# Optimization experiments

Measured on AMD Instinct MI355X. Metric: run time of the kernel, lower is better.

## Reference

```python
import jax, jax.numpy as jnp
import numpy as np

B, P, F = 128, 196, 2048   # batch, num_pixels, feature_dim
E, H, V = 512, 512, 10000  # embed_dim, hidden_dim, vocab_size
T = 32                     # max caption length


def setup_inputs() -> dict:
    key = jax.random.key(0)
    ks = jax.random.split(key, 12)
    s_e, s_h, s_f = 1.0 / np.sqrt(E), 1.0 / np.sqrt(H), 1.0 / np.sqrt(F)
    return {
        "features": jax.random.normal(ks[0], (B, P, F), jnp.float32),
        "captions": jax.random.randint(ks[1], (B, T), 0, V),
        # embedding table (init uniform(-0.1, 0.1) in the original)
        "emb_W": jax.random.uniform(ks[2], (V, E), jnp.float32, -0.1, 0.1),
        # LSTMCell params (PyTorch layout: [4H, in] with gate order i,f,g,o)
        "W_ih": jax.random.uniform(ks[3], (4 * H, E), jnp.float32, -s_h, s_h),
        "W_hh": jax.random.uniform(ks[4], (4 * H, H), jnp.float32, -s_h, s_h),
        "b_ih": jax.random.uniform(ks[5], (4 * H,), jnp.float32, -s_h, s_h),
        "b_hh": jax.random.uniform(ks[6], (4 * H,), jnp.float32, -s_h, s_h),
        # init_h / init_c linear layers: feature_dim -> hidden_dim
        "Wh": jax.random.uniform(ks[7], (H, F), jnp.float32, -s_f, s_f),
        "bh": jax.random.uniform(ks[8], (H,), jnp.float32, -s_f, s_f),
        "Wc": jax.random.uniform(ks[9], (H, F), jnp.float32, -s_f, s_f),
        "bc": jax.random.uniform(ks[10], (H,), jnp.float32, -s_f, s_f),
        # output projection (uniform(-0.1, 0.1) weights, zero bias)
        "fc_W": jax.random.uniform(ks[11], (V, H), jnp.float32, -0.1, 0.1),
        "fc_b": jnp.zeros((V,), jnp.float32),
    }


def _decode(features, captions, emb_W, W_ih, W_hh, b_ih, b_hh, Wh, bh, Wc, bc, fc_W, fc_b):
    # init hidden state from mean pooled features
    mean_feat = features.mean(axis=1)                       # [B, F]
    h0 = mean_feat @ Wh.T + bh                              # [B, H]
    c0 = mean_feat @ Wc.T + bc                              # [B, H]

    embeds = emb_W[captions]                                # [B, T, E]
    # x-side gate preactivations for all steps at once: [T-1, B, 4H]
    x_gates = jnp.einsum('bte,ge->tbg', embeds[:, :-1, :], W_ih) + (b_ih + b_hh)

    def step(carry, xg):
        h, c = carry
        gates = xg + h @ W_hh.T                             # [B, 4H]
        i, f, g, o = jnp.split(gates, 4, axis=-1)
        i, f, o = jax.nn.sigmoid(i), jax.nn.sigmoid(f), jax.nn.sigmoid(o)
        g = jnp.tanh(g)
        c_new = f * c + i * g
        h_new = o * jnp.tanh(c_new)
        return (h_new, c_new), h_new

    _, hs = jax.lax.scan(step, (h0, c0), x_gates)           # hs: [T-1, B, H]
    hs = jnp.swapaxes(hs, 0, 1)                             # [B, T-1, H]
    # dropout is identity in eval mode; fc applied per step == batched matmul
    return jnp.einsum('bth,vh->btv', hs, fc_W) + fc_b       # [B, T-1, V]


def reference(features, captions, emb_W, W_ih, W_hh, b_ih, b_hh, Wh, bh, Wc, bc, fc_W, fc_b):
    return _decode(features, captions, emb_W, W_ih, W_hh, b_ih, b_hh, Wh, bh, Wc, bc, fc_W, fc_b)
```

## Files before the change

kernel.cpp:

```cpp
#include <hip/hip_runtime.h>
#include <hip/hip_bf16.h>
#include <cstddef>

#define Bz 128
#define Pz 196
#define Fz 2048
#define Ez 512
#define Hz 512
#define Vz 10000
#define Tz 32
#define TM 31
#define Mrows (Bz * TM)
#define G4 (4 * Hz)
#define NPAD 10112

typedef __attribute__((ext_vector_type(8))) short bf16x8;
typedef __attribute__((ext_vector_type(4))) float f32x4;

__device__ __forceinline__ void gload_lds16(const void* g, void* l) {
    __builtin_amdgcn_global_load_lds(
        (const __attribute__((address_space(1))) unsigned int*)g,
        (__attribute__((address_space(3))) unsigned int*)l, 16, 0, 0);
}
__device__ __forceinline__ ushort f2b(float x) {
    __hip_bfloat16 b = __float2bfloat16(x);
    return *reinterpret_cast<ushort*>(&b);
}
__device__ __forceinline__ float b2f(ushort u) {
    __hip_bfloat16 b = *reinterpret_cast<__hip_bfloat16*>(&u);
    return __bfloat162float(b);
}

__global__ __launch_bounds__(256) void meanpool(const float* __restrict__ feat,
                                                float* __restrict__ mean) {
    int idx = blockIdx.x * 256 + threadIdx.x;
    int b = idx >> 9;
    int q = idx & 511;
    const float4* base = reinterpret_cast<const float4*>(feat) +
                         (size_t)b * Pz * (Fz / 4) + q;
    float4 acc = {0.f, 0.f, 0.f, 0.f};
    for (int p = 0; p < Pz; ++p) {
        float4 v = base[(size_t)p * (Fz / 4)];
        acc.x += v.x; acc.y += v.y; acc.z += v.z; acc.w += v.w;
    }
    const float s = 1.0f / (float)Pz;
    acc.x *= s; acc.y *= s; acc.z *= s; acc.w *= s;
    reinterpret_cast<float4*>(mean)[idx] = acc;
}

__global__ __launch_bounds__(256) void gather_cvt_emb(const float* __restrict__ emb,
                                                      const int* __restrict__ cap,
                                                      ushort* __restrict__ out) {
    int idx = blockIdx.x * 256 + threadIdx.x;
    if (idx >= Mrows * (Ez / 4)) return;
    int m = idx >> 7, kq = idx & 127;
    int b = m / TM;
    int t = m - b * TM;
    int row = cap[b * Tz + t];
    float4 v = reinterpret_cast<const float4*>(emb + (size_t)row * Ez)[kq];
    ushort4 o = {f2b(v.x), f2b(v.y), f2b(v.z), f2b(v.w)};
    reinterpret_cast<ushort4*>(out + (size_t)m * Ez)[kq] = o;
}

__global__ __launch_bounds__(256) void permute_wih(const float* __restrict__ W,
                                                   const float* __restrict__ b1,
                                                   const float* __restrict__ b2,
                                                   ushort* __restrict__ WP,
                                                   float* __restrict__ bP) {
    int idx = blockIdx.x * 256 + threadIdx.x;
    int o = idx >> 7, kq = idx & 127;
    int j = o >> 2, g = o & 3;
    int in = g * Hz + j;
    float4 v = reinterpret_cast<const float4*>(W + (size_t)in * Ez)[kq];
    ushort4 u = {f2b(v.x), f2b(v.y), f2b(v.z), f2b(v.w)};
    reinterpret_cast<ushort4*>(WP + (size_t)o * Ez)[kq] = u;
    if (kq == 0) bP[o] = b1[in] + b2[in];
}

__global__ __launch_bounds__(256) void permute_whh(const float* __restrict__ W,
                                                   ushort* __restrict__ Whi) {
    int idx = blockIdx.x * 256 + threadIdx.x;
    int o = idx >> 7, kq = idx & 127;
    int j = o >> 2, g = o & 3;
    int in = g * Hz + j;
    float4 v = reinterpret_cast<const float4*>(W + (size_t)in * Hz)[kq];
    ushort4 h = {f2b(v.x), f2b(v.y), f2b(v.z), f2b(v.w)};
    reinterpret_cast<ushort4*>(Whi + (size_t)o * Hz)[kq] = h;
}

__global__ __launch_bounds__(256) void cvt_bf16_pad4(const float* __restrict__ s,
                                                     ushort* __restrict__ d,
                                                     int n4src, int n4dst) {
    int i = blockIdx.x * 256 + threadIdx.x;
    if (i >= n4dst) return;
    ushort4 o;
    if (i < n4src) {
        float4 v = reinterpret_cast<const float4*>(s)[i];
        o.x = f2b(v.x); o.y = f2b(v.y); o.z = f2b(v.z); o.w = f2b(v.w);
    } else {
        o.x = o.y = o.z = o.w = 0;
    }
    reinterpret_cast<ushort4*>(d)[i] = o;
}

__global__ __launch_bounds__(256) void initk(
    const float* __restrict__ mean,
    const float* __restrict__ Wh, const float* __restrict__ Wc,
    float* __restrict__ partial)
{
    __shared__ float As[64][33];
    __shared__ float Bs2[64][33];
    const int n0 = blockIdx.x * 64;
    const int m0 = blockIdx.y * 64;
    const int kz = blockIdx.z;
    const int tid = threadIdx.x;
    const int tx = tid & 15, ty = tid >> 4;
    float acc[4][4] = {};

    for (int k0 = kz * 256; k0 < kz * 256 + 256; k0 += 32) {
#pragma unroll
        for (int i = 0; i < 2; ++i) {
            int e  = tid + i * 256;
            int r  = e >> 3;
            int cc = (e & 7) << 2;
            float4 va = *reinterpret_cast<const float4*>(
                mean + (size_t)(m0 + r) * Fz + k0 + cc);
            As[r][cc + 0] = va.x; As[r][cc + 1] = va.y;
            As[r][cc + 2] = va.z; As[r][cc + 3] = va.w;
            int n = n0 + r;
            const float* Brow = (n < Hz) ? (Wh + (size_t)n * Fz)
                                         : (Wc + (size_t)(n - Hz) * Fz);
            float4 vb = *reinterpret_cast<const float4*>(Brow + k0 + cc);
            Bs2[r][cc + 0] = vb.x; Bs2[r][cc + 1] = vb.y;
            Bs2[r][cc + 2] = vb.z; Bs2[r][cc + 3] = vb.w;
        }
        __syncthreads();
#pragma unroll
        for (int kk = 0; kk < 32; ++kk) {
            float a[4], bb[4];
#pragma unroll
            for (int i = 0; i < 4; ++i) a[i] = As[ty * 4 + i][kk];
#pragma unroll
            for (int j = 0; j < 4; ++j) bb[j] = Bs2[tx * 4 + j][kk];
#pragma unroll
            for (int i = 0; i < 4; ++i)
#pragma unroll
                for (int j = 0; j < 4; ++j)
                    acc[i][j] += a[i] * bb[j];
        }
        __syncthreads();
    }
#pragma unroll
    for (int i = 0; i < 4; ++i)
#pragma unroll
        for (int j = 0; j < 4; ++j)
            partial[((size_t)kz * 128 + m0 + ty * 4 + i) * 1024 + n0 + tx * 4 + j]
                = acc[i][j];
}

__global__ __launch_bounds__(256) void init_reduce(
    const float* __restrict__ partial,
    const float* __restrict__ bh, const float* __restrict__ bc,
    ushort* __restrict__ haHi, ushort* __restrict__ haLo,
    float* __restrict__ c0f)
{
    int idx = blockIdx.x * 256 + threadIdx.x;
    if (idx >= 128 * 1024) return;
    int m = idx >> 10, n = idx & 1023;
    float s = 0.f;
#pragma unroll
    for (int z = 0; z < 8; ++z)
        s += partial[((size_t)z * 128 + m) * 1024 + n];
    if (n < Hz) {
        s += bh[n];
        ushort hh = f2b(s);
        haHi[(size_t)m * Hz + n] = hh;
        haLo[(size_t)m * Hz + n] = f2b(s - b2f(hh));
    } else {
        c0f[(size_t)m * Hz + (n - Hz)] = s + bc[n - Hz];
    }
}

__global__ __launch_bounds__(256) void gemm_mfma(
    const ushort* __restrict__ A,
    const ushort* __restrict__ B,
    const float* __restrict__ bias,
    float* __restrict__ C,
    int Nb, int ldc, int K)
{
    __shared__ short Al[128 * 32];
    __shared__ short Bl[128 * 32];
    const int tid  = threadIdx.x;
    const int w    = tid >> 6;
    const int lane = tid & 63;

    const int nwg  = gridDim.x * gridDim.y;
    int orig = blockIdx.y * gridDim.x + blockIdx.x;
    int q = nwg >> 3, r = nwg & 7;
    int xcd = orig & 7, local = orig >> 3;
    int wgid = (xcd < r ? xcd * (q + 1) : r * (q + 1) + (xcd - r) * q) + local;
    const int m0 = (wgid / gridDim.x) * 128;
    const int n0 = (wgid % gridDim.x) * 128;
    const int wr = w >> 1, wc = w & 1;

    f32x4 acc[4][4] = {};

    const int srow = w * 32 + (lane >> 2);
    const int scol = (lane & 3) * 16;
    const char* Ag = (const char*)(A + (size_t)(m0 + srow) * K) + scol;
    const char* Bg = (const char*)(B + (size_t)(n0 + srow) * K) + scol;
    const size_t rstep = (size_t)16 * K * 2;
    short* Alb = Al + (w * 32) * 32;
    short* Blb = Bl + (w * 32) * 32;

    const int ko = (lane >> 4) * 8;
    const int fr = lane & 15;

    for (int k0 = 0; k0 < K; k0 += 32) {
        const size_t kb = (size_t)k0 * 2;
        gload_lds16(Ag + kb,         Alb);
        gload_lds16(Ag + kb + rstep, Alb + 16 * 32);
        gload_lds16(Bg + kb,         Blb);
        gload_lds16(Bg + kb + rstep, Blb + 16 * 32);
        __syncthreads();

        bf16x8 af[4], bf[4];
#pragma unroll
        for (int i = 0; i < 4; ++i)
            af[i] = *reinterpret_cast<const bf16x8*>(&Al[(wr * 64 + i * 16 + fr) * 32 + ko]);
#pragma unroll
        for (int j = 0; j < 4; ++j)
            bf[j] = *reinterpret_cast<const bf16x8*>(&Bl[(wc * 64 + j * 16 + fr) * 32 + ko]);
#pragma unroll
        for (int i = 0; i < 4; ++i)
#pragma unroll
            for (int j = 0; j < 4; ++j)
                acc[i][j] = __builtin_amdgcn_mfma_f32_16x16x32_bf16(
                    af[i], bf[j], acc[i][j], 0, 0, 0);
        __syncthreads();
    }

    const int r0 = (lane >> 4) * 4;
#pragma unroll
    for (int i = 0; i < 4; ++i) {
        int row = m0 + wr * 64 + i * 16 + r0;
#pragma unroll
        for (int j = 0; j < 4; ++j) {
            int col = n0 + wc * 64 + j * 16 + fr;
            if (col < Nb) {
                float bb = bias ? bias[col] : 0.f;
#pragma unroll
                for (int rr = 0; rr < 4; ++rr)
                    C[(size_t)(row + rr) * ldc + col] = acc[i][j][rr] + bb;
            }
        }
    }
}

__global__ __launch_bounds__(128) void lstm_step2(
    const float* __restrict__ xg,
    const ushort* __restrict__ Whi,
    const ushort* __restrict__ Ah,  const ushort* __restrict__ Alo,
    ushort* __restrict__ Oh, ushort* __restrict__ Ol,
    float* __restrict__ cst, ushort* __restrict__ hsb, int t)
{
    __shared__ float Cl[64][17];

    const int tid  = threadIdx.x;
    const int w    = tid >> 6;
    const int lane = tid & 63;
    const int fr   = lane & 15;
    const int hi4  = lane >> 4;
    const int n0   = blockIdx.x * 16;
    const int j0   = n0 >> 2;
    const int mb   = blockIdx.y * 64;
    const int m0w  = mb + w * 32;

    f32x4 acc[2] = {};

    const ushort* Bp  = Whi + (size_t)(n0 + fr) * Hz;
    const ushort* Ap0 = Ah  + (size_t)(m0w + fr) * Hz;
    const ushort* Ap1 = Ah  + (size_t)(m0w + 16 + fr) * Hz;
    const ushort* Lp0 = Alo + (size_t)(m0w + fr) * Hz;
    const ushort* Lp1 = Alo + (size_t)(m0w + 16 + fr) * Hz;

#pragma unroll
    for (int kc = 0; kc < 16; ++kc) {
        const size_t koff = (size_t)kc * 32 + hi4 * 8;
        bf16x8 bv  = *reinterpret_cast<const bf16x8*>(Bp  + koff);
        bf16x8 ah0 = *reinterpret_cast<const bf16x8*>(Ap0 + koff);
        bf16x8 ah1 = *reinterpret_cast<const bf16x8*>(Ap1 + koff);
        bf16x8 al0 = *reinterpret_cast<const bf16x8*>(Lp0 + koff);
        bf16x8 al1 = *reinterpret_cast<const bf16x8*>(Lp1 + koff);
        acc[0] = __builtin_amdgcn_mfma_f32_16x16x32_bf16(ah0, bv, acc[0], 0, 0, 0);
        acc[1] = __builtin_amdgcn_mfma_f32_16x16x32_bf16(ah1, bv, acc[1], 0, 0, 0);
        acc[0] = __builtin_amdgcn_mfma_f32_16x16x32_bf16(al0, bv, acc[0], 0, 0, 0);
        acc[1] = __builtin_amdgcn_mfma_f32_16x16x32_bf16(al1, bv, acc[1], 0, 0, 0);
    }

#pragma unroll
    for (int i = 0; i < 2; ++i)
#pragma unroll
        for (int r = 0; r < 4; ++r)
            Cl[w * 32 + i * 16 + hi4 * 4 + r][fr] = acc[i][r];
    __syncthreads();

    {
        const int lm = tid >> 1;
        const int m  = mb + lm;
        const int hp = (tid & 1) * 2;
        const float* xr = xg + ((size_t)m * TM + t) * G4 + n0 + 4 * hp;
        float4 x0 = *reinterpret_cast<const float4*>(xr);
        float4 x1 = *reinterpret_cast<const float4*>(xr + 4);
        float2 cc = *reinterpret_cast<const float2*>(cst + (size_t)m * Hz + j0 + hp);

        float gi0 = Cl[lm][4 * hp + 0] + x0.x;
        float gf0 = Cl[lm][4 * hp + 1] + x0.y;
        float gg0 = Cl[lm][4 * hp + 2] + x0.z;
        float go0 = Cl[lm][4 * hp + 3] + x0.w;
        float gi1 = Cl[lm][4 * hp + 4] + x1.x;
        float gf1 = Cl[lm][4 * hp + 5] + x1.y;
        float gg1 = Cl[lm][4 * hp + 6] + x1.z;
        float go1 = Cl[lm][4 * hp + 7] + x1.w;

        float i0 = 1.f / (1.f + expf(-gi0));
        float f0 = 1.f / (1.f + expf(-gf0));
        float g0 = tanhf(gg0);
        float o0 = 1.f / (1.f + expf(-go0));
        float i1 = 1.f / (1.f + expf(-gi1));
        float f1 = 1.f / (1.f + expf(-gf1));
        float g1 = tanhf(gg1);
        float o1 = 1.f / (1.f + expf(-go1));

        float cn0 = f0 * cc.x + i0 * g0;
        float cn1 = f1 * cc.y + i1 * g1;
        float h0v = o0 * tanhf(cn0);
        float h1v = o1 * tanhf(cn1);

        float2 cno = {cn0, cn1};
        *reinterpret_cast<float2*>(cst + (size_t)m * Hz + j0 + hp) = cno;

        ushort hh0 = f2b(h0v), hh1 = f2b(h1v);
        ushort hl0 = f2b(h0v - b2f(hh0)), hl1 = f2b(h1v - b2f(hh1));
        uint uh = (uint)hh0 | ((uint)hh1 << 16);
        uint ul = (uint)hl0 | ((uint)hl1 << 16);
        *reinterpret_cast<uint*>(Oh + (size_t)m * Hz + j0 + hp) = uh;
        *reinterpret_cast<uint*>(Ol + (size_t)m * Hz + j0 + hp) = ul;
        *reinterpret_cast<uint*>(hsb + ((size_t)m * TM + t) * Hz + j0 + hp) = uh;
    }
}

extern "C" void kernel_launch(void* const* d_in, const int* in_sizes, int n_in,
                              void* d_out, int out_size, void* d_ws, size_t ws_size,
                              hipStream_t stream) {
    const float* features = (const float*)d_in[0];
    const int*   captions = (const int*)d_in[1];
    const float* emb_W    = (const float*)d_in[2];
    const float* W_ih     = (const float*)d_in[3];
    const float* W_hh     = (const float*)d_in[4];
    const float* b_ih     = (const float*)d_in[5];
    const float* b_hh     = (const float*)d_in[6];
    const float* Wh       = (const float*)d_in[7];
    const float* bh       = (const float*)d_in[8];
    const float* Wc       = (const float*)d_in[9];
    const float* bc       = (const float*)d_in[10];
    const float* fc_W     = (const float*)d_in[11];
    const float* fc_b     = (const float*)d_in[12];
    float* out = (float*)d_out;

    float* w    = (float*)d_ws;
    float* mean = w;
    float* xg   = mean + Bz * Fz;
    float* partial = xg;
    float* c0f  = xg + (size_t)Mrows * G4;
    float* bP   = c0f + Bz * Hz;
    ushort* embg = (ushort*)(bP + G4);
    ushort* WihP = embg + (size_t)Mrows * Ez;
    ushort* Whi  = WihP + (size_t)G4 * Ez;
    ushort* fcWb = Whi + (size_t)G4 * Hz;
    ushort* hsb  = fcWb + (size_t)NPAD * Hz;
    ushort* haHi = hsb + (size_t)Mrows * Hz;
    ushort* haLo = haHi + Bz * Hz;
    ushort* hbHi = haLo + Bz * Hz;
    ushort* hbLo = hbHi + Bz * Hz;

    meanpool<<<(Bz * Fz / 4) / 256, 256, 0, stream>>>(features, mean);
    gather_cvt_emb<<<(Mrows * (Ez / 4) + 255) / 256, 256, 0, stream>>>(emb_W, captions, embg);
    permute_wih<<<(G4 * (Ez / 4)) / 256, 256, 0, stream>>>(W_ih, b_ih, b_hh, WihP, bP);
    permute_whh<<<(G4 * (Hz / 4)) / 256, 256, 0, stream>>>(W_hh, Whi);
    cvt_bf16_pad4<<<(NPAD * Hz / 4 + 255) / 256, 256, 0, stream>>>(
        fc_W, fcWb, Vz * Hz / 4, NPAD * Hz / 4);

    initk<<<dim3(16, 2, 8), 256, 0, stream>>>(mean, Wh, Wc, partial);
    init_reduce<<<(128 * 1024) / 256, 256, 0, stream>>>(
        partial, bh, bc, haHi, haLo, c0f);

    gemm_mfma<<<dim3(G4 / 128, Mrows / 128), 256, 0, stream>>>(
        embg, WihP, bP, xg, G4, G4, Ez);

    for (int t = 0; t < TM; ++t) {
        const ushort* ih = (t & 1) ? hbHi : haHi;
        const ushort* il = (t & 1) ? hbLo : haLo;
        ushort* oh = (t & 1) ? haHi : hbHi;
        ushort* ol = (t & 1) ? haLo : hbLo;
        lstm_step2<<<dim3(G4 / 16, 2), 128, 0, stream>>>(
            xg, Whi, ih, il, oh, ol, c0f, hsb, t);
    }

    gemm_mfma<<<dim3(NPAD / 128, Mrows / 128), 256, 0, stream>>>(
        hsb, fcWb, fc_b, out, Vz, Vz, Hz);
}
```

Baseline: 484.2 us.

## Double-buffer LDS in GEMM and split LSTM step into single-wave blocks

The GEMM kernel now keeps two LDS buffers, so the global-to-LDS load for the next K tile is issued before the MFMAs on the current tile, with one barrier per iteration instead of two. This aims to hide global load latency behind compute, at the cost of doubling shared memory per block, which may lower occupancy. The LSTM step kernel now uses 64-thread blocks covering 32 rows, with a grid twice as tall. That doubles the block count for the latency-bound recurrent step and shrinks each block's barrier scope.

```diff
diff --git a/kernel.cpp b/kernel.cpp
--- a/kernel.cpp
+++ b/kernel.cpp
@@ -188,8 +188,8 @@
     float* __restrict__ C,
     int Nb, int ldc, int K)
 {
-    __shared__ short Al[128 * 32];
-    __shared__ short Bl[128 * 32];
+    __shared__ short Al[2][128 * 32];
+    __shared__ short Bl[2][128 * 32];
     const int tid  = threadIdx.x;
     const int w    = tid >> 6;
     const int lane = tid & 63;
@@ -210,27 +210,36 @@
     const char* Ag = (const char*)(A + (size_t)(m0 + srow) * K) + scol;
     const char* Bg = (const char*)(B + (size_t)(n0 + srow) * K) + scol;
     const size_t rstep = (size_t)16 * K * 2;
-    short* Alb = Al + (w * 32) * 32;
-    short* Blb = Bl + (w * 32) * 32;
+    const int ldsb = (w * 32) * 32;
 
     const int ko = (lane >> 4) * 8;
     const int fr = lane & 15;
-
-    for (int k0 = 0; k0 < K; k0 += 32) {
-        const size_t kb = (size_t)k0 * 2;
-        gload_lds16(Ag + kb,         Alb);
-        gload_lds16(Ag + kb + rstep, Alb + 16 * 32);
-        gload_lds16(Bg + kb,         Blb);
-        gload_lds16(Bg + kb + rstep, Blb + 16 * 32);
-        __syncthreads();
-
+    const int nk = K >> 5;
+
+    {
+        gload_lds16(Ag,         Al[0] + ldsb);
+        gload_lds16(Ag + rstep, Al[0] + ldsb + 16 * 32);
+        gload_lds16(Bg,         Bl[0] + ldsb);
+        gload_lds16(Bg + rstep, Bl[0] + ldsb + 16 * 32);
+    }
+    __syncthreads();
+
+    int cur = 0;
+    for (int k = 0; k < nk; ++k) {
+        if (k + 1 < nk) {
+            const size_t kb = (size_t)(k + 1) * 64;
+            gload_lds16(Ag + kb,         Al[cur ^ 1] + ldsb);
+            gload_lds16(Ag + kb + rstep, Al[cur ^ 1] + ldsb + 16 * 32);
+            gload_lds16(Bg + kb,         Bl[cur ^ 1] + ldsb);
+            gload_lds16(Bg + kb + rstep, Bl[cur ^ 1] + ldsb + 16 * 32);
+        }
         bf16x8 af[4], bf[4];
 #pragma unroll
         for (int i = 0; i < 4; ++i)
-            af[i] = *reinterpret_cast<const bf16x8*>(&Al[(wr * 64 + i * 16 + fr) * 32 + ko]);
+            af[i] = *reinterpret_cast<const bf16x8*>(&Al[cur][(wr * 64 + i * 16 + fr) * 32 + ko]);
 #pragma unroll
         for (int j = 0; j < 4; ++j)
-            bf[j] = *reinterpret_cast<const bf16x8*>(&Bl[(wc * 64 + j * 16 + fr) * 32 + ko]);
+            bf[j] = *reinterpret_cast<const bf16x8*>(&Bl[cur][(wc * 64 + j * 16 + fr) * 32 + ko]);
 #pragma unroll
         for (int i = 0; i < 4; ++i)
 #pragma unroll
@@ -238,6 +247,7 @@
                 acc[i][j] = __builtin_amdgcn_mfma_f32_16x16x32_bf16(
                     af[i], bf[j], acc[i][j], 0, 0, 0);
         __syncthreads();
+        cur ^= 1;
     }
 
     const int r0 = (lane >> 4) * 4;
@@ -257,24 +267,22 @@
     }
 }
 
-__global__ __launch_bounds__(128) void lstm_step2(
+__global__ __launch_bounds__(64) void lstm_step2(
     const float* __restrict__ xg,
     const ushort* __restrict__ Whi,
     const ushort* __restrict__ Ah,  const ushort* __restrict__ Alo,
     ushort* __restrict__ Oh, ushort* __restrict__ Ol,
     float* __restrict__ cst, ushort* __restrict__ hsb, int t)
 {
-    __shared__ float Cl[64][17];
+    __shared__ float Cl[32][17];
 
     const int tid  = threadIdx.x;
-    const int w    = tid >> 6;
     const int lane = tid & 63;
     const int fr   = lane & 15;
     const int hi4  = lane >> 4;
     const int n0   = blockIdx.x * 16;
     const int j0   = n0 >> 2;
-    const int mb   = blockIdx.y * 64;
-    const int m0w  = mb + w * 32;
+    const int m0w  = blockIdx.y * 32;
 
     f32x4 acc[2] = {};
 
@@ -302,12 +310,12 @@
     for (int i = 0; i < 2; ++i)
 #pragma unroll
         for (int r = 0; r < 4; ++r)
-            Cl[w * 32 + i * 16 + hi4 * 4 + r][fr] = acc[i][r];
+            Cl[i * 16 + hi4 * 4 + r][fr] = acc[i][r];
     __syncthreads();
 
     {
         const int lm = tid >> 1;
-        const int m  = mb + lm;
+        const int m  = m0w + lm;
         const int hp = (tid & 1) * 2;
         const float* xr = xg + ((size_t)m * TM + t) * G4 + n0 + 4 * hp;
         float4 x0 = *reinterpret_cast<const float4*>(xr);
@@ -403,7 +411,7 @@
         const ushort* il = (t & 1) ? hbLo : haLo;
         ushort* oh = (t & 1) ? haHi : hbHi;
         ushort* ol = (t & 1) ? haLo : hbLo;
-        lstm_step2<<<dim3(G4 / 16, 2), 128, 0, stream>>>(
+        lstm_step2<<<dim3(G4 / 16, 4), 64, 0, stream>>>(
             xg, Whi, ih, il, oh, ol, c0f, hsb, t);
     }
 
```

Result: no change. 482.1 us (-0.4%).
